# Optimization experiments

Measured on AMD Instinct MI355X. Metric: run time of the kernel, lower is better.

The kernel has to match this reference:

```python
import jax, jax.numpy as jnp
import numpy as np

B, R, S, M, L = 16, 64, 128, 64, 128  # batch, regions, src_dim, message_dim, max_latent
E = R * R - R  # 4032 directed edges (all ordered pairs, no self loops)


def _edge_indices():
    s, t = np.meshgrid(np.arange(R), np.arange(R), indexing='ij')
    mask = s != t
    return s[mask].astype(np.int64), t[mask].astype(np.int64)


def setup_inputs() -> dict:
    key = jax.random.key(0)
    ks = jax.random.split(key, 8)
    src_np, tgt_np = _edge_indices()
    xav_ms = float(np.sqrt(6.0 / (M + S)))  # xavier_uniform bound for (M,S) matrices
    small = 0.02  # torch inits add_w/gain_w to zeros; use small random for non-trivial outputs
    return {
        'source': jax.random.normal(ks[0], (B, R, S), jnp.float32),
        'mean_w': jax.random.uniform(ks[1], (E, M, S), jnp.float32, -xav_ms, xav_ms),
        'mean_b': jnp.zeros((E, M), jnp.float32),
        'logstd_w': jax.random.uniform(ks[2], (E, M, S), jnp.float32, -xav_ms, xav_ms),
        'logstd_b': jnp.zeros((E, M), jnp.float32),
        'add_w': small * jax.random.normal(ks[3], (E, L, M), jnp.float32),
        'gain_w': small * jax.random.normal(ks[4], (E, L, M), jnp.float32),
        'src_idx': jnp.asarray(src_np),
        'tgt_idx': jnp.asarray(tgt_np),
        'deterministic': 1,
    }


def reference(source, mean_w, mean_b, logstd_w, logstd_b, add_w, gain_w,
              src_idx, tgt_idx, deterministic):
    B_, E_ = source.shape[0], src_idx.shape[0]
    # gather source features per edge: [B, E, S]
    src = source[:, src_idx, :]
    # per-edge grouped GEMMs
    mean = jnp.einsum('bes,ems->bem', src, mean_w) + mean_b      # [B, E, M]
    logstd = jnp.einsum('bes,ems->bem', src, logstd_w) + logstd_b
    # deterministic path: msg = mean (softplus(std) only used when sampling)
    msg = mean
    add = jnp.einsum('bem,elm->bel', msg, add_w)                  # [B, E, L]
    gain = jnp.einsum('bem,elm->bel', msg, gain_w)
    # scatter-add over target regions
    inc_add = jnp.zeros((B_, R, L), source.dtype).at[:, tgt_idx].add(add)
    inc_gain = jnp.zeros((B_, R, L), source.dtype).at[:, tgt_idx].add(gain)
    # scatter (unique flat indices) into dense [B, R, R, M] message tensors
    flat = src_idx * R + tgt_idx
    def scat(x):
        return jnp.zeros((B_, R * R, M), source.dtype).at[:, flat].set(x).reshape(B_, R, R, M)
    return inc_add, inc_gain, scat(mean), scat(logstd), scat(msg)
```

## Files before the change

kernel.cpp:

```cpp
#include <hip/hip_runtime.h>

#define BB 16
#define RR 64
#define SS 128
#define MM 64
#define LL 128
#define EE 4032

#define OUT3_OFF 262144
#define ARR_SZ   4194304

__global__ __launch_bounds__(256) void k_zero(float* __restrict__ out) {
  int tid = blockIdx.x * 256 + threadIdx.x;
  if (tid < 262144) { out[tid] = 0.0f; return; }
  int idx = tid - 262144;
  int a = idx >> 16;
  int r = idx & 65535;
  int b = r >> 12;
  int d = (r >> 6) & 63;
  int m = r & 63;
  out[OUT3_OFF + (size_t)a * ARR_SZ + (size_t)b * 262144 + d * 4160 + m] = 0.0f;
}

__global__ __launch_bounds__(256) void k_edge(
    const float* __restrict__ source,
    const float* __restrict__ mean_w,
    const float* __restrict__ mean_b,
    const float* __restrict__ logstd_w,
    const float* __restrict__ logstd_b,
    const int* __restrict__ src_idx,
    const int* __restrict__ tgt_idx,
    float* __restrict__ out)
{
  __shared__ float lds_src[BB * 132];
  __shared__ float lds_mean[BB * 64];
  __shared__ float lds_logstd[BB * 64];
  const int e = blockIdx.x;
  const int tid = threadIdx.x;
  const int sidx = src_idx[e];
  const int tidx = tgt_idx[e];

  #pragma unroll
  for (int f0 = 0; f0 < 2; ++f0) {
    int f = tid + f0 * 256;
    int b = f >> 5, s4 = f & 31;
    float4 v = *(const float4*)(source + ((size_t)b * (RR * SS) + (size_t)sidx * SS + s4 * 4));
    *(float4*)(lds_src + b * 132 + s4 * 4) = v;
  }
  __syncthreads();

  const int m = tid >> 2;
  const int sq = tid & 3;
  float accm[BB], accl[BB];
  #pragma unroll
  for (int b = 0; b < BB; ++b) { accm[b] = 0.0f; accl[b] = 0.0f; }

  const float* wmp = mean_w   + ((size_t)e * (MM * SS) + (size_t)m * SS);
  const float* wlp = logstd_w + ((size_t)e * (MM * SS) + (size_t)m * SS);
  #pragma unroll
  for (int k = 0; k < 8; ++k) {
    const int soff = sq * 4 + k * 16;
    float4 a = *(const float4*)(wmp + soff);
    float4 c = *(const float4*)(wlp + soff);
    #pragma unroll
    for (int b = 0; b < BB; ++b) {
      float4 sv = *(const float4*)(lds_src + b * 132 + soff);
      accm[b] = fmaf(a.x, sv.x, fmaf(a.y, sv.y, fmaf(a.z, sv.z, fmaf(a.w, sv.w, accm[b]))));
      accl[b] = fmaf(c.x, sv.x, fmaf(c.y, sv.y, fmaf(c.z, sv.z, fmaf(c.w, sv.w, accl[b]))));
    }
  }
  #pragma unroll
  for (int b = 0; b < BB; ++b) {
    accm[b] += __shfl_xor(accm[b], 1);
    accm[b] += __shfl_xor(accm[b], 2);
    accl[b] += __shfl_xor(accl[b], 1);
    accl[b] += __shfl_xor(accl[b], 2);
  }
  const float bm = mean_b[e * MM + m];
  const float bl = logstd_b[e * MM + m];
  #pragma unroll
  for (int j = 0; j < 4; ++j) {
    int b = sq * 4 + j;
    lds_mean[b * 64 + m]   = accm[b] + bm;
    lds_logstd[b * 64 + m] = accl[b] + bl;
  }
  __syncthreads();

  float* out3 = out + OUT3_OFF;
  float* out4 = out3 + ARR_SZ;
  float* out5 = out4 + ARR_SZ;
  const size_t rowbase = (size_t)(sidx * RR + tidx) * MM;
  const int b = tid >> 4, m4 = tid & 15;
  float4 vm = *(float4*)(lds_mean + b * 64 + m4 * 4);
  float4 vl = *(float4*)(lds_logstd + b * 64 + m4 * 4);
  size_t o = (size_t)b * (RR * RR * MM) + rowbase + m4 * 4;
  *(float4*)(out3 + o) = vm;
  *(float4*)(out4 + o) = vl;
  *(float4*)(out5 + o) = vm;
}

__global__ __launch_bounds__(256) void k_inc(
    const float* __restrict__ add_w,
    const float* __restrict__ gain_w,
    float* __restrict__ out)
{
  __shared__ float lds_mean[BB * 64];
  const int g = blockIdx.x;
  const int tt = g / 18;
  const int r = g % 18;
  const int lh = r / 9;
  const int c = r % 9;
  const int tid = threadIdx.x;
  const int l_loc = tid >> 2;
  const int mq = tid & 3;
  const int l = lh * 64 + l_loc;

  float acca[BB], accg[BB];
  #pragma unroll
  for (int b = 0; b < BB; ++b) { acca[b] = 0.0f; accg[b] = 0.0f; }

  const float* out3 = out + OUT3_OFF;
  for (int j = 0; j < 7; ++j) {
    const int si = c * 7 + j;
    const int s = si + (si >= tt ? 1 : 0);
    const int e = s * 63 + (tt > s ? tt - 1 : tt);
    __syncthreads();
    {
      int b = tid >> 4, m4 = tid & 15;
      *(float4*)(lds_mean + b * 64 + m4 * 4) =
          *(const float4*)(out3 + ((size_t)b * 262144 + (size_t)(s * 64 + tt) * 64 + m4 * 4));
    }
    __syncthreads();
    const float* wa = add_w  + ((size_t)e * (LL * MM) + (size_t)l * MM + mq * 16);
    const float* wg = gain_w + ((size_t)e * (LL * MM) + (size_t)l * MM + mq * 16);
    #pragma unroll
    for (int i = 0; i < 4; ++i) {
      float4 a  = *(const float4*)(wa + i * 4);
      float4 gq = *(const float4*)(wg + i * 4);
      #pragma unroll
      for (int b = 0; b < BB; ++b) {
        float4 mv = *(const float4*)(lds_mean + b * 64 + mq * 16 + i * 4);
        acca[b] = fmaf(a.x,  mv.x, fmaf(a.y,  mv.y, fmaf(a.z,  mv.z, fmaf(a.w,  mv.w, acca[b]))));
        accg[b] = fmaf(gq.x, mv.x, fmaf(gq.y, mv.y, fmaf(gq.z, mv.z, fmaf(gq.w, mv.w, accg[b]))));
      }
    }
  }
  #pragma unroll
  for (int b = 0; b < BB; ++b) {
    acca[b] += __shfl_xor(acca[b], 1);
    acca[b] += __shfl_xor(acca[b], 2);
    accg[b] += __shfl_xor(accg[b], 1);
    accg[b] += __shfl_xor(accg[b], 2);
  }
  float* inc_add  = out;
  float* inc_gain = out + 131072;
  #pragma unroll
  for (int jj = 0; jj < 4; ++jj) {
    int b = mq * 4 + jj;
    size_t o = (size_t)b * (RR * LL) + (size_t)tt * LL + l;
    atomicAdd(inc_add + o, acca[b]);
    atomicAdd(inc_gain + o, accg[b]);
  }
}

extern "C" void kernel_launch(void* const* d_in, const int* in_sizes, int n_in,
                              void* d_out, int out_size, void* d_ws, size_t ws_size,
                              hipStream_t stream) {
  const float* source   = (const float*)d_in[0];
  const float* mean_w   = (const float*)d_in[1];
  const float* mean_b   = (const float*)d_in[2];
  const float* logstd_w = (const float*)d_in[3];
  const float* logstd_b = (const float*)d_in[4];
  const float* add_w    = (const float*)d_in[5];
  const float* gain_w   = (const float*)d_in[6];
  const int*   src_idx  = (const int*)d_in[7];
  const int*   tgt_idx  = (const int*)d_in[8];
  float* out = (float*)d_out;

  k_zero<<<1792, 256, 0, stream>>>(out);
  k_edge<<<EE, 256, 0, stream>>>(source, mean_w, mean_b, logstd_w, logstd_b,
                                 src_idx, tgt_idx, out);
  k_inc<<<1152, 256, 0, stream>>>(add_w, gain_w, out);
}
```

Before: 479.3 us.

## Software-pipeline weight and message loads in edge and incoming kernels

In k_edge, the first two weight float4s are loaded before the LDS barrier, and each later chunk is loaded two iterations ahead, so global latency overlaps the FMA work. In k_inc, the per-edge mean vector and add/gain weights for the next edge are prefetched into registers while the current edge is computed. A double-buffered LDS tile there lets one barrier per iteration replace two. This raises register pressure, which could lower occupancy.

```diff
diff --git a/kernel.cpp b/kernel.cpp
--- a/kernel.cpp
+++ b/kernel.cpp
@@ -47,27 +47,39 @@
     float4 v = *(const float4*)(source + ((size_t)b * (RR * SS) + (size_t)sidx * SS + s4 * 4));
     *(float4*)(lds_src + b * 132 + s4 * 4) = v;
   }
-  __syncthreads();
 
   const int m = tid >> 2;
   const int sq = tid & 3;
+
+  const float* wmp = mean_w   + ((size_t)e * (MM * SS) + (size_t)m * SS) + sq * 4;
+  const float* wlp = logstd_w + ((size_t)e * (MM * SS) + (size_t)m * SS) + sq * 4;
+
+  float4 a0 = *(const float4*)(wmp + 0);
+  float4 c0 = *(const float4*)(wlp + 0);
+  float4 a1 = *(const float4*)(wmp + 16);
+  float4 c1 = *(const float4*)(wlp + 16);
+
+  __syncthreads();
+
   float accm[BB], accl[BB];
   #pragma unroll
   for (int b = 0; b < BB; ++b) { accm[b] = 0.0f; accl[b] = 0.0f; }
 
-  const float* wmp = mean_w   + ((size_t)e * (MM * SS) + (size_t)m * SS);
-  const float* wlp = logstd_w + ((size_t)e * (MM * SS) + (size_t)m * SS);
   #pragma unroll
   for (int k = 0; k < 8; ++k) {
+    float4 a2 = {}, c2 = {};
+    if (k < 6) {
+      a2 = *(const float4*)(wmp + (k + 2) * 16);
+      c2 = *(const float4*)(wlp + (k + 2) * 16);
+    }
     const int soff = sq * 4 + k * 16;
-    float4 a = *(const float4*)(wmp + soff);
-    float4 c = *(const float4*)(wlp + soff);
     #pragma unroll
     for (int b = 0; b < BB; ++b) {
       float4 sv = *(const float4*)(lds_src + b * 132 + soff);
-      accm[b] = fmaf(a.x, sv.x, fmaf(a.y, sv.y, fmaf(a.z, sv.z, fmaf(a.w, sv.w, accm[b]))));
-      accl[b] = fmaf(c.x, sv.x, fmaf(c.y, sv.y, fmaf(c.z, sv.z, fmaf(c.w, sv.w, accl[b]))));
-    }
+      accm[b] = fmaf(a0.x, sv.x, fmaf(a0.y, sv.y, fmaf(a0.z, sv.z, fmaf(a0.w, sv.w, accm[b]))));
+      accl[b] = fmaf(c0.x, sv.x, fmaf(c0.y, sv.y, fmaf(c0.z, sv.z, fmaf(c0.w, sv.w, accl[b]))));
+    }
+    a0 = a1; c0 = c1; a1 = a2; c1 = c2;
   }
   #pragma unroll
   for (int b = 0; b < BB; ++b) {
@@ -104,7 +116,7 @@
     const float* __restrict__ gain_w,
     float* __restrict__ out)
 {
-  __shared__ float lds_mean[BB * 64];
+  __shared__ float lds_mean[2][BB * 64];
   const int g = blockIdx.x;
   const int tt = g / 18;
   const int r = g % 18;
@@ -114,34 +126,63 @@
   const int l_loc = tid >> 2;
   const int mq = tid & 3;
   const int l = lh * 64 + l_loc;
+  const int b16 = tid >> 4, m4 = tid & 15;
+
+  const float* out3 = out + OUT3_OFF;
 
   float acca[BB], accg[BB];
   #pragma unroll
   for (int b = 0; b < BB; ++b) { acca[b] = 0.0f; accg[b] = 0.0f; }
 
-  const float* out3 = out + OUT3_OFF;
-  for (int j = 0; j < 7; ++j) {
-    const int si = c * 7 + j;
+  float4 mv_n;
+  float4 wa_n[4], wg_n[4];
+  {
+    const int si = c * 7;
     const int s = si + (si >= tt ? 1 : 0);
     const int e = s * 63 + (tt > s ? tt - 1 : tt);
-    __syncthreads();
-    {
-      int b = tid >> 4, m4 = tid & 15;
-      *(float4*)(lds_mean + b * 64 + m4 * 4) =
-          *(const float4*)(out3 + ((size_t)b * 262144 + (size_t)(s * 64 + tt) * 64 + m4 * 4));
-    }
-    __syncthreads();
+    mv_n = *(const float4*)(out3 + ((size_t)b16 * 262144 + (size_t)(s * 64 + tt) * 64 + m4 * 4));
     const float* wa = add_w  + ((size_t)e * (LL * MM) + (size_t)l * MM + mq * 16);
     const float* wg = gain_w + ((size_t)e * (LL * MM) + (size_t)l * MM + mq * 16);
     #pragma unroll
     for (int i = 0; i < 4; ++i) {
-      float4 a  = *(const float4*)(wa + i * 4);
-      float4 gq = *(const float4*)(wg + i * 4);
+      wa_n[i] = *(const float4*)(wa + i * 4);
+      wg_n[i] = *(const float4*)(wg + i * 4);
+    }
+  }
+
+  #pragma unroll
+  for (int j = 0; j < 7; ++j) {
+    float4 mv = mv_n;
+    float4 wa_c[4], wg_c[4];
+    #pragma unroll
+    for (int i = 0; i < 4; ++i) { wa_c[i] = wa_n[i]; wg_c[i] = wg_n[i]; }
+
+    *(float4*)(&lds_mean[j & 1][b16 * 64 + m4 * 4]) = mv;
+    __syncthreads();
+
+    if (j < 6) {
+      const int si2 = c * 7 + j + 1;
+      const int s2 = si2 + (si2 >= tt ? 1 : 0);
+      const int e2 = s2 * 63 + (tt > s2 ? tt - 1 : tt);
+      mv_n = *(const float4*)(out3 + ((size_t)b16 * 262144 + (size_t)(s2 * 64 + tt) * 64 + m4 * 4));
+      const float* wa2 = add_w  + ((size_t)e2 * (LL * MM) + (size_t)l * MM + mq * 16);
+      const float* wg2 = gain_w + ((size_t)e2 * (LL * MM) + (size_t)l * MM + mq * 16);
+      #pragma unroll
+      for (int i = 0; i < 4; ++i) {
+        wa_n[i] = *(const float4*)(wa2 + i * 4);
+        wg_n[i] = *(const float4*)(wg2 + i * 4);
+      }
+    }
+
+    #pragma unroll
+    for (int i = 0; i < 4; ++i) {
+      float4 a  = wa_c[i];
+      float4 gq = wg_c[i];
       #pragma unroll
       for (int b = 0; b < BB; ++b) {
-        float4 mv = *(const float4*)(lds_mean + b * 64 + mq * 16 + i * 4);
-        acca[b] = fmaf(a.x,  mv.x, fmaf(a.y,  mv.y, fmaf(a.z,  mv.z, fmaf(a.w,  mv.w, acca[b]))));
-        accg[b] = fmaf(gq.x, mv.x, fmaf(gq.y, mv.y, fmaf(gq.z, mv.z, fmaf(gq.w, mv.w, accg[b]))));
+        float4 mvv = *(const float4*)(&lds_mean[j & 1][b * 64 + mq * 16 + i * 4]);
+        acca[b] = fmaf(a.x,  mvv.x, fmaf(a.y,  mvv.y, fmaf(a.z,  mvv.z, fmaf(a.w,  mvv.w, acca[b]))));
+        accg[b] = fmaf(gq.x, mvv.x, fmaf(gq.y, mvv.y, fmaf(gq.z, mvv.z, fmaf(gq.w, mvv.w, accg[b]))));
       }
     }
   }
```

Measured after the change: 479.1 us. Within noise of the previous version (-0.0%).
